# Kernel tuning notes

Measured on AMD Instinct MI355X. Metric: run time of the kernel, lower is better.

## Reference

```python
import jax, jax.numpy as jnp
import numpy as np

B, N, D = 8, 1024, 1024

def setup_inputs() -> dict:
    key = jax.random.key(0)
    k1, k2, k3, k4, k5 = jax.random.split(key, 5)
    x = jax.random.normal(k1, (B, N, D), dtype=jnp.float32)
    y = jax.random.normal(k2, (B, N, D), dtype=jnp.float32)
    adj = jax.random.uniform(k3, (B, N, N), dtype=jnp.float32)
    adj_sumrow = jnp.sum(adj, axis=-1, keepdims=True)  # [B, N, 1], row-sum normalizer
    W = jax.random.normal(k4, (D, D), dtype=jnp.float32) * (1.0 / np.sqrt(D))
    b = jax.random.normal(k5, (D,), dtype=jnp.float32) * 0.02
    return {"x": x, "y": y, "adj": adj, "adj_sumrow": adj_sumrow, "W": W, "b": b}

def reference(x, y, adj, adj_sumrow, W, b):
    # GraphConvolutionCustom: project neighbor features, aggregate via dense adj,
    # normalize by row-sum, add bias and residual input x; then ReLU.
    # Dropout is identity in eval mode (training=False).
    support = jnp.einsum('bnd,de->bne', y, W)          # [B, N, D]
    agg = jnp.matmul(adj, support) / adj_sumrow        # [B, N, D]
    out = jax.nn.relu(agg + b + x)
    return out
```

## Files before the change

kernel.cpp:

```cpp
#include <hip/hip_runtime.h>
#include <hip/hip_bf16.h>
#include <stdint.h>


typedef float  f32x4  __attribute__((ext_vector_type(4)));
typedef __bf16 bf16x8 __attribute__((ext_vector_type(8)));

__device__ __forceinline__ unsigned short f2bf(float f) {
  union { float f; unsigned int u; } c; c.f = f;
  unsigned int u = c.u;
  u += 0x7FFFu + ((u >> 16) & 1u);
  return (unsigned short)(u >> 16);
}

__device__ __forceinline__ void async_cp16(const void* g, void* l) {
  __builtin_amdgcn_global_load_lds(
      (const __attribute__((address_space(1))) unsigned int*)g,
      (__attribute__((address_space(3))) unsigned int*)l, 16, 0, 0);
}

__device__ __forceinline__ void bar() { asm volatile("s_barrier" ::: "memory"); }
#define VMCNT(n) asm volatile("s_waitcnt vmcnt(" #n ")" ::: "memory")


__global__ __launch_bounds__(256) void k_prep(
    const float4* __restrict__ y4, const float4* __restrict__ a4,
    ushort4* __restrict__ yb, ushort4* __restrict__ ab,
    const float* __restrict__ W, unsigned short* __restrict__ Wt)
{
  const int bid = blockIdx.x;
  if (bid < 2048) {
    const bool isY = bid < 1024;
    const float4* __restrict__ src = isY ? y4 : a4;
    ushort4* __restrict__ dst = isY ? yb : ab;
    int idx = (bid & 1023) * 256 + (int)threadIdx.x;
#pragma unroll
    for (int it = 0; it < 8; ++it, idx += 262144) {
      const float4 v = src[idx];
      ushort4 p;
      p.x = f2bf(v.x); p.y = f2bf(v.y); p.z = f2bf(v.z); p.w = f2bf(v.w);
      dst[idx] = p;
    }
  } else {
    __shared__ float t[64][65];
    const int id = bid - 2048;
    const int n0 = (id & 15) * 64, k0 = (id >> 4) * 64;
    const int tx = threadIdx.x & 63, ty = threadIdx.x >> 6;
#pragma unroll
    for (int r = ty; r < 64; r += 4)
      t[r][tx] = W[(size_t)(k0 + r) * 1024 + n0 + tx];
    __syncthreads();
#pragma unroll
    for (int r = ty; r < 64; r += 4)
      Wt[(size_t)(n0 + r) * 1024 + k0 + tx] = f2bf(t[tx][r]);
  }
}


__device__ __forceinline__ void stageA(
    const unsigned short* __restrict__ A, int sA, int m0, int k0, int c,
    unsigned short* la, int wave, int rg, int colo)
{
#pragma unroll
  for (int s = 0; s < 2; ++s) {
    const int t = wave * 2 + s;
    const int row0 = (t >> 2) * 64 + c * 32 + (t & 3) * 8;
    async_cp16(A + (size_t)(m0 + row0 + rg) * sA + k0 + colo, la + row0 * 64);
  }
}

__device__ __forceinline__ void stageB(
    const unsigned short* __restrict__ Bt, int sB, int n0, int k0,
    unsigned short* lb, int wave, int rg, int colo)
{
#pragma unroll
  for (int s = 0; s < 2; ++s) {
    const int t = wave * 2 + s;
    const int row0 = t * 8;
    async_cp16(Bt + (size_t)(n0 + row0 + rg) * sB + k0 + colo, lb + row0 * 64);
  }
}

__device__ __forceinline__ void readA(
    const unsigned short* la, bf16x8 af[2][2], int wm, int mh, int quad, int l16)
{
#pragma unroll
  for (int h = 0; h < 2; ++h)
#pragma unroll
    for (int i = 0; i < 2; ++i) {
      const int r = wm + mh * 32 + i * 16 + l16;
      af[h][i] = *(const bf16x8*)(la + r * 64 + ((h * 4 + quad + r) & 7) * 8);
    }
}

__device__ __forceinline__ void readB(
    const unsigned short* lb, bf16x8 bfr[2][2], int wn, int nh, int quad, int l16)
{
#pragma unroll
  for (int h = 0; h < 2; ++h)
#pragma unroll
    for (int j = 0; j < 2; ++j) {
      const int r = wn + nh * 32 + j * 16 + l16;
      bfr[h][j] = *(const bf16x8*)(lb + r * 64 + ((h * 4 + quad + r) & 7) * 8);
    }
}

__device__ __forceinline__ void quad8(
    bf16x8 af[2][2], bf16x8 bfr[2][2], f32x4 acc[4][4], int mh, int nh)
{
  __builtin_amdgcn_s_setprio(1);
#pragma unroll
  for (int h = 0; h < 2; ++h)
#pragma unroll
    for (int i = 0; i < 2; ++i)
#pragma unroll
      for (int j = 0; j < 2; ++j)
        acc[mh * 2 + i][nh * 2 + j] = __builtin_amdgcn_mfma_f32_16x16x32_bf16(
            af[h][i], bfr[h][j], acc[mh * 2 + i][nh * 2 + j], 0, 0, 0);
  __builtin_amdgcn_s_setprio(0);
}

__device__ __forceinline__ void gemm256x128(
    const unsigned short* __restrict__ A,  int sA,
    const unsigned short* __restrict__ Bt, int sB,
    int m0, int n0, f32x4 acc[4][4], unsigned short* lsm, int tid)
{
  const int lane = tid & 63, wave = tid >> 6;
  const int wm = (wave >> 1) * 64, wn = (wave & 1) * 64;
  const int quad = lane >> 4, l16 = lane & 15;
  const int rg = lane >> 3;
  const int colo = (((lane & 7) - rg) & 7) * 8;

  bf16x8 af[2][2], bfr[2][2];

  stageA(A, sA, m0, 0, 0, lsm, wave, rg, colo);
  stageB(Bt, sB, n0, 0, lsm + 16384, wave, rg, colo);
  stageA(A, sA, m0, 0, 1, lsm, wave, rg, colo);

#pragma unroll 1
  for (int T = 0; T < 15; ++T) {
    const unsigned short* la = lsm + (T & 1) * 24576;
    const unsigned short* lb = la + 16384;
    unsigned short* na = lsm + ((T + 1) & 1) * 24576;
    unsigned short* nb = na + 16384;
    const int nk = (T + 1) * 64;

    stageA(A, sA, m0, nk, 0, na, wave, rg, colo);
    VMCNT(4); bar();
    readA(la, af, wm, 0, quad, l16);
    readB(lb, bfr, wn, 0, quad, l16);
    quad8(af, bfr, acc, 0, 0);

    stageB(Bt, sB, n0, nk, nb, wave, rg, colo);
    readB(lb, bfr, wn, 1, quad, l16);
    quad8(af, bfr, acc, 0, 1);

    stageA(A, sA, m0, nk, 1, na, wave, rg, colo);
    VMCNT(6); bar();
    readA(la, af, wm, 1, quad, l16);
    quad8(af, bfr, acc, 1, 1);

    readB(lb, bfr, wn, 0, quad, l16);
    quad8(af, bfr, acc, 1, 0);
  }

  {
    const unsigned short* la = lsm + 24576;
    const unsigned short* lb = la + 16384;
    VMCNT(2); bar();
    readA(la, af, wm, 0, quad, l16);
    readB(lb, bfr, wn, 0, quad, l16);
    quad8(af, bfr, acc, 0, 0);
    readB(lb, bfr, wn, 1, quad, l16);
    quad8(af, bfr, acc, 0, 1);
    VMCNT(0); bar();
    readA(la, af, wm, 1, quad, l16);
    quad8(af, bfr, acc, 1, 1);
    readB(lb, bfr, wn, 0, quad, l16);
    quad8(af, bfr, acc, 1, 0);
  }
}

__device__ __forceinline__ void zero_acc(f32x4 acc[4][4]) {
#pragma unroll
  for (int i = 0; i < 4; ++i)
#pragma unroll
    for (int j = 0; j < 4; ++j)
#pragma unroll
      for (int r = 0; r < 4; ++r) acc[i][j][r] = 0.0f;
}


__global__ __launch_bounds__(512, 2) void k_gemm1(
    const unsigned short* __restrict__ Wt,
    const unsigned short* __restrict__ Ybf,
    unsigned short* __restrict__ Sup2)
{
  __shared__ __align__(16) unsigned short lsm[49152];
  const int tid = threadIdx.x;
  const int xcd = blockIdx.x & 7, slot = blockIdx.x >> 3;
  const int m0 = (slot >> 3) * 256;
  const int n0 = (xcd * 8 + (slot & 7)) * 128;

  f32x4 acc[4][4];
  zero_acc(acc);
  gemm256x128(Wt, 1024, Ybf, 1024, m0, n0, acc, lsm, tid);

  const int lane = tid & 63, wave = tid >> 6;
  const int wm = (wave >> 1) * 64, wn = (wave & 1) * 64;
  const int quad = lane >> 4, l16 = lane & 15;
#pragma unroll
  for (int mi = 0; mi < 4; ++mi) {
    const int mb = m0 + wm + mi * 16 + quad * 4;
#pragma unroll
    for (int r = 0; r < 4; ++r) {
      unsigned short* row = Sup2 + ((size_t)(mb + r) << 13);
#pragma unroll
      for (int nj = 0; nj < 4; ++nj)
        row[n0 + wn + nj * 16 + l16] = f2bf(acc[mi][nj][r]);
    }
  }
}


__global__ __launch_bounds__(512, 2) void k_gemm2(
    const unsigned short* __restrict__ AdjBf,
    const unsigned short* __restrict__ Sup2,
    const float* __restrict__ x,
    const float* __restrict__ sumrow,
    const float* __restrict__ bias,
    float* __restrict__ out)
{
  __shared__ __align__(16) unsigned short lsm[49152];
  const int tid = threadIdx.x;
  const int b = blockIdx.x & 7, slot = blockIdx.x >> 3;
  const int m0 = (slot >> 3) * 256, n0 = (slot & 7) * 128;

  f32x4 acc[4][4];
  zero_acc(acc);
  gemm256x128(AdjBf + ((size_t)b << 20), 1024,
              Sup2 + ((size_t)b << 10), 8192,
              m0, n0, acc, lsm, tid);

  const float* xb = x   + ((size_t)b << 20);
  float*       ob = out + ((size_t)b << 20);
  const float* sr = sumrow + ((size_t)b << 10);
  const int lane = tid & 63, wave = tid >> 6;
  const int wm = (wave >> 1) * 64, wn = (wave & 1) * 64;
  const int quad = lane >> 4, l16 = lane & 15;

  float bv[4];
#pragma unroll
  for (int nj = 0; nj < 4; ++nj) bv[nj] = bias[n0 + wn + nj * 16 + l16];

#pragma unroll
  for (int mi = 0; mi < 4; ++mi) {
    const int mb = m0 + wm + mi * 16 + quad * 4;
#pragma unroll
    for (int r = 0; r < 4; ++r) {
      const int m = mb + r;
      const float inv = 1.0f / sr[m];
#pragma unroll
      for (int nj = 0; nj < 4; ++nj) {
        const int n = n0 + wn + nj * 16 + l16;
        const size_t idx = (((size_t)m) << 10) + n;
        float v = acc[mi][nj][r] * inv + bv[nj] + xb[idx];
        ob[idx] = fmaxf(v, 0.0f);
      }
    }
  }
}


extern "C" void kernel_launch(void* const* d_in, const int* in_sizes, int n_in,
                              void* d_out, int out_size, void* d_ws, size_t ws_size,
                              hipStream_t stream) {
  const float* x      = (const float*)d_in[0];
  const float* y      = (const float*)d_in[1];
  const float* adj    = (const float*)d_in[2];
  const float* sumrow = (const float*)d_in[3];
  const float* W      = (const float*)d_in[4];
  const float* bias   = (const float*)d_in[5];
  float* out = (float*)d_out;

  char* ws = (char*)d_ws;
  unsigned short* ybf   = (unsigned short*)(ws);
  unsigned short* adjbf = (unsigned short*)(ws + ((size_t)16 << 20));
  unsigned short* wt    = (unsigned short*)(ws + ((size_t)32 << 20));
  unsigned short* sup2  = (unsigned short*)(ws + ((size_t)34 << 20));

  k_prep<<<dim3(2304), dim3(256), 0, stream>>>(
      (const float4*)y, (const float4*)adj, (ushort4*)ybf, (ushort4*)adjbf, W, wt);
  k_gemm1<<<dim3(256), dim3(512), 0, stream>>>(wt, ybf, sup2);
  k_gemm2<<<dim3(256), dim3(512), 0, stream>>>(adjbf, sup2, x, sumrow, bias, out);
}
```

Before: 197.6 us.

## Fuse adjacency bf16 conversion into the first GEMM's main loop

Moves the fp32-to-bf16 conversion of the adjacency matrix out of the prep kernel and into k_gemm1. Each k-iteration of the GEMM loop now loads one float4 of adj and writes its bf16 copy, so this memory-bound traffic overlaps with MFMA compute. The GEMM pipeline is inlined into the kernel to interleave the extra loads. It adds register pressure and extra vmcnt interactions: the extra load may shift the counts the hard-coded VMCNT waits rely on.

```diff
diff --git a/kernel.cpp b/kernel.cpp
--- a/kernel.cpp
+++ b/kernel.cpp
@@ -24,26 +24,22 @@
 
 
 __global__ __launch_bounds__(256) void k_prep(
-    const float4* __restrict__ y4, const float4* __restrict__ a4,
-    ushort4* __restrict__ yb, ushort4* __restrict__ ab,
+    const float4* __restrict__ y4, ushort4* __restrict__ yb,
     const float* __restrict__ W, unsigned short* __restrict__ Wt)
 {
   const int bid = blockIdx.x;
-  if (bid < 2048) {
-    const bool isY = bid < 1024;
-    const float4* __restrict__ src = isY ? y4 : a4;
-    ushort4* __restrict__ dst = isY ? yb : ab;
-    int idx = (bid & 1023) * 256 + (int)threadIdx.x;
+  if (bid < 1024) {
+    int idx = bid * 256 + (int)threadIdx.x;
 #pragma unroll
     for (int it = 0; it < 8; ++it, idx += 262144) {
-      const float4 v = src[idx];
+      const float4 v = y4[idx];
       ushort4 p;
       p.x = f2bf(v.x); p.y = f2bf(v.y); p.z = f2bf(v.z); p.w = f2bf(v.w);
-      dst[idx] = p;
+      yb[idx] = p;
     }
   } else {
     __shared__ float t[64][65];
-    const int id = bid - 2048;
+    const int id = bid - 1024;
     const int n0 = (id & 15) * 64, k0 = (id >> 4) * 64;
     const int tx = threadIdx.x & 63, ty = threadIdx.x >> 6;
 #pragma unroll
@@ -118,6 +114,15 @@
         acc[mh * 2 + i][nh * 2 + j] = __builtin_amdgcn_mfma_f32_16x16x32_bf16(
             af[h][i], bfr[h][j], acc[mh * 2 + i][nh * 2 + j], 0, 0, 0);
   __builtin_amdgcn_s_setprio(0);
+}
+
+__device__ __forceinline__ void zero_acc(f32x4 acc[4][4]) {
+#pragma unroll
+  for (int i = 0; i < 4; ++i)
+#pragma unroll
+    for (int j = 0; j < 4; ++j)
+#pragma unroll
+      for (int r = 0; r < 4; ++r) acc[i][j][r] = 0.0f;
 }
 
 __device__ __forceinline__ void gemm256x128(
@@ -163,7 +168,6 @@
     readB(lb, bfr, wn, 0, quad, l16);
     quad8(af, bfr, acc, 1, 0);
   }
-
   {
     const unsigned short* la = lsm + 24576;
     const unsigned short* lb = la + 16384;
@@ -181,20 +185,13 @@
   }
 }
 
-__device__ __forceinline__ void zero_acc(f32x4 acc[4][4]) {
-#pragma unroll
-  for (int i = 0; i < 4; ++i)
-#pragma unroll
-    for (int j = 0; j < 4; ++j)
-#pragma unroll
-      for (int r = 0; r < 4; ++r) acc[i][j][r] = 0.0f;
-}
-
 
 __global__ __launch_bounds__(512, 2) void k_gemm1(
     const unsigned short* __restrict__ Wt,
     const unsigned short* __restrict__ Ybf,
-    unsigned short* __restrict__ Sup2)
+    unsigned short* __restrict__ Sup2,
+    const float4* __restrict__ AdjF,
+    ushort4* __restrict__ AdjBf)
 {
   __shared__ __align__(16) unsigned short lsm[49152];
   const int tid = threadIdx.x;
@@ -202,13 +199,73 @@
   const int m0 = (slot >> 3) * 256;
   const int n0 = (xcd * 8 + (slot & 7)) * 128;
 
-  f32x4 acc[4][4];
-  zero_acc(acc);
-  gemm256x128(Wt, 1024, Ybf, 1024, m0, n0, acc, lsm, tid);
+  const int cvBase = blockIdx.x * 8192 + tid;
 
   const int lane = tid & 63, wave = tid >> 6;
   const int wm = (wave >> 1) * 64, wn = (wave & 1) * 64;
   const int quad = lane >> 4, l16 = lane & 15;
+  const int rg = lane >> 3;
+  const int colo = (((lane & 7) - rg) & 7) * 8;
+
+  f32x4 acc[4][4];
+  zero_acc(acc);
+  bf16x8 af[2][2], bfr[2][2];
+
+  stageA(Wt, 1024, m0, 0, 0, lsm, wave, rg, colo);
+  stageB(Ybf, 1024, n0, 0, lsm + 16384, wave, rg, colo);
+  stageA(Wt, 1024, m0, 0, 1, lsm, wave, rg, colo);
+
+#pragma unroll 1
+  for (int T = 0; T < 15; ++T) {
+    const unsigned short* la = lsm + (T & 1) * 24576;
+    const unsigned short* lb = la + 16384;
+    unsigned short* na = lsm + ((T + 1) & 1) * 24576;
+    unsigned short* nb = na + 16384;
+    const int nk = (T + 1) * 64;
+
+    stageA(Wt, 1024, m0, nk, 0, na, wave, rg, colo);
+    VMCNT(4); bar();
+    readA(la, af, wm, 0, quad, l16);
+    readB(lb, bfr, wn, 0, quad, l16);
+    quad8(af, bfr, acc, 0, 0);
+
+    stageB(Ybf, 1024, n0, nk, nb, wave, rg, colo);
+    const float4 cv = AdjF[cvBase + T * 512];
+    readB(lb, bfr, wn, 1, quad, l16);
+    quad8(af, bfr, acc, 0, 1);
+
+    stageA(Wt, 1024, m0, nk, 1, na, wave, rg, colo);
+    VMCNT(6); bar();
+    readA(la, af, wm, 1, quad, l16);
+    quad8(af, bfr, acc, 1, 1);
+
+    readB(lb, bfr, wn, 0, quad, l16);
+    quad8(af, bfr, acc, 1, 0);
+    ushort4 pk;
+    pk.x = f2bf(cv.x); pk.y = f2bf(cv.y); pk.z = f2bf(cv.z); pk.w = f2bf(cv.w);
+    AdjBf[cvBase + T * 512] = pk;
+  }
+
+  {
+    const unsigned short* la = lsm + 24576;
+    const unsigned short* lb = la + 16384;
+    const float4 cv = AdjF[cvBase + 15 * 512];
+    VMCNT(2); bar();
+    readA(la, af, wm, 0, quad, l16);
+    readB(lb, bfr, wn, 0, quad, l16);
+    quad8(af, bfr, acc, 0, 0);
+    readB(lb, bfr, wn, 1, quad, l16);
+    quad8(af, bfr, acc, 0, 1);
+    VMCNT(0); bar();
+    readA(la, af, wm, 1, quad, l16);
+    quad8(af, bfr, acc, 1, 1);
+    readB(lb, bfr, wn, 0, quad, l16);
+    quad8(af, bfr, acc, 1, 0);
+    ushort4 pk;
+    pk.x = f2bf(cv.x); pk.y = f2bf(cv.y); pk.z = f2bf(cv.z); pk.w = f2bf(cv.w);
+    AdjBf[cvBase + 15 * 512] = pk;
+  }
+
 #pragma unroll
   for (int mi = 0; mi < 4; ++mi) {
     const int mb = m0 + wm + mi * 16 + quad * 4;
@@ -289,8 +346,9 @@
   unsigned short* wt    = (unsigned short*)(ws + ((size_t)32 << 20));
   unsigned short* sup2  = (unsigned short*)(ws + ((size_t)34 << 20));
 
-  k_prep<<<dim3(2304), dim3(256), 0, stream>>>(
-      (const float4*)y, (const float4*)adj, (ushort4*)ybf, (ushort4*)adjbf, W, wt);
-  k_gemm1<<<dim3(256), dim3(512), 0, stream>>>(wt, ybf, sup2);
+  k_prep<<<dim3(1280), dim3(256), 0, stream>>>(
+      (const float4*)y, (ushort4*)ybf, W, wt);
+  k_gemm1<<<dim3(256), dim3(512), 0, stream>>>(
+      wt, ybf, sup2, (const float4*)adj, (ushort4*)adjbf);
   k_gemm2<<<dim3(256), dim3(512), 0, stream>>>(adjbf, sup2, x, sumrow, bias, out);
 }
```

Result: no change. 197.7 us (+0.0%).

## Overlap adjacency bf16 conversion with first GEMM using extra waves

Applied to the files above, without the earlier changes.

Removes the adj fp32-to-bf16 conversion from the prep kernel. That work now runs on four extra waves added to each first-GEMM workgroup, which grows to 768 threads. The goal is to hide the memory-bound conversion behind the MMA-bound projection GEMM instead of running it serially. In exchange, the launch bounds lose the two-blocks-per-CU hint. The converter waves also issue s_barrier every iteration, which couples their progress to the GEMM waves' barriers and may stall either side.

```diff
diff --git a/kernel.cpp b/kernel.cpp
--- a/kernel.cpp
+++ b/kernel.cpp
@@ -24,26 +24,22 @@
 
 
 __global__ __launch_bounds__(256) void k_prep(
-    const float4* __restrict__ y4, const float4* __restrict__ a4,
-    ushort4* __restrict__ yb, ushort4* __restrict__ ab,
+    const float4* __restrict__ y4, ushort4* __restrict__ yb,
     const float* __restrict__ W, unsigned short* __restrict__ Wt)
 {
   const int bid = blockIdx.x;
-  if (bid < 2048) {
-    const bool isY = bid < 1024;
-    const float4* __restrict__ src = isY ? y4 : a4;
-    ushort4* __restrict__ dst = isY ? yb : ab;
-    int idx = (bid & 1023) * 256 + (int)threadIdx.x;
+  if (bid < 1024) {
+    int idx = bid * 256 + (int)threadIdx.x;
 #pragma unroll
     for (int it = 0; it < 8; ++it, idx += 262144) {
-      const float4 v = src[idx];
+      const float4 v = y4[idx];
       ushort4 p;
       p.x = f2bf(v.x); p.y = f2bf(v.y); p.z = f2bf(v.z); p.w = f2bf(v.w);
-      dst[idx] = p;
+      yb[idx] = p;
     }
   } else {
     __shared__ float t[64][65];
-    const int id = bid - 2048;
+    const int id = bid - 1024;
     const int n0 = (id & 15) * 64, k0 = (id >> 4) * 64;
     const int tx = threadIdx.x & 63, ty = threadIdx.x >> 6;
 #pragma unroll
@@ -163,7 +159,6 @@
     readB(lb, bfr, wn, 0, quad, l16);
     quad8(af, bfr, acc, 1, 0);
   }
-
   {
     const unsigned short* la = lsm + 24576;
     const unsigned short* lb = la + 16384;
@@ -191,33 +186,51 @@
 }
 
 
-__global__ __launch_bounds__(512, 2) void k_gemm1(
+__global__ __launch_bounds__(768) void k_gemm1(
     const unsigned short* __restrict__ Wt,
     const unsigned short* __restrict__ Ybf,
-    unsigned short* __restrict__ Sup2)
+    unsigned short* __restrict__ Sup2,
+    const float4* __restrict__ AdjF,
+    ushort4* __restrict__ AdjBf)
 {
   __shared__ __align__(16) unsigned short lsm[49152];
   const int tid = threadIdx.x;
-  const int xcd = blockIdx.x & 7, slot = blockIdx.x >> 3;
-  const int m0 = (slot >> 3) * 256;
-  const int n0 = (xcd * 8 + (slot & 7)) * 128;
-
-  f32x4 acc[4][4];
-  zero_acc(acc);
-  gemm256x128(Wt, 1024, Ybf, 1024, m0, n0, acc, lsm, tid);
-
-  const int lane = tid & 63, wave = tid >> 6;
-  const int wm = (wave >> 1) * 64, wn = (wave & 1) * 64;
-  const int quad = lane >> 4, l16 = lane & 15;
-#pragma unroll
-  for (int mi = 0; mi < 4; ++mi) {
-    const int mb = m0 + wm + mi * 16 + quad * 4;
-#pragma unroll
-    for (int r = 0; r < 4; ++r) {
-      unsigned short* row = Sup2 + ((size_t)(mb + r) << 13);
-#pragma unroll
-      for (int nj = 0; nj < 4; ++nj)
-        row[n0 + wn + nj * 16 + l16] = f2bf(acc[mi][nj][r]);
+
+  if (tid < 512) {
+    const int xcd = blockIdx.x & 7, slot = blockIdx.x >> 3;
+    const int m0 = (slot >> 3) * 256;
+    const int n0 = (xcd * 8 + (slot & 7)) * 128;
+
+    f32x4 acc[4][4];
+    zero_acc(acc);
+    gemm256x128(Wt, 1024, Ybf, 1024, m0, n0, acc, lsm, tid);
+
+    const int lane = tid & 63, wave = tid >> 6;
+    const int wm = (wave >> 1) * 64, wn = (wave & 1) * 64;
+    const int quad = lane >> 4, l16 = lane & 15;
+#pragma unroll
+    for (int mi = 0; mi < 4; ++mi) {
+      const int mb = m0 + wm + mi * 16 + quad * 4;
+#pragma unroll
+      for (int r = 0; r < 4; ++r) {
+        unsigned short* row = Sup2 + ((size_t)(mb + r) << 13);
+#pragma unroll
+        for (int nj = 0; nj < 4; ++nj)
+          row[n0 + wn + nj * 16 + l16] = f2bf(acc[mi][nj][r]);
+      }
+    }
+  } else {
+    const int ct = blockIdx.x * 256 + (tid - 512);
+    float4 cur = AdjF[ct];
+#pragma unroll 1
+    for (int it = 0; it < 32; ++it) {
+      float4 nxt = cur;
+      if (it < 31) nxt = AdjF[ct + (it + 1) * 65536];
+      ushort4 p;
+      p.x = f2bf(cur.x); p.y = f2bf(cur.y); p.z = f2bf(cur.z); p.w = f2bf(cur.w);
+      AdjBf[ct + it * 65536] = p;
+      cur = nxt;
+      bar();
     }
   }
 }
@@ -289,8 +302,9 @@
   unsigned short* wt    = (unsigned short*)(ws + ((size_t)32 << 20));
   unsigned short* sup2  = (unsigned short*)(ws + ((size_t)34 << 20));
 
-  k_prep<<<dim3(2304), dim3(256), 0, stream>>>(
-      (const float4*)y, (const float4*)adj, (ushort4*)ybf, (ushort4*)adjbf, W, wt);
-  k_gemm1<<<dim3(256), dim3(512), 0, stream>>>(wt, ybf, sup2);
+  k_prep<<<dim3(1280), dim3(256), 0, stream>>>(
+      (const float4*)y, (ushort4*)ybf, W, wt);
+  k_gemm1<<<dim3(256), dim3(768), 0, stream>>>(
+      wt, ybf, sup2, (const float4*)adj, (ushort4*)adjbf);
   k_gemm2<<<dim3(256), dim3(512), 0, stream>>>(adjbf, sup2, x, sumrow, bias, out);
 }
```

Measured after the change: 192.8 us. 1.03x faster.
